# Kernel optimization log

Hardware: AMD Instinct MI355X
Metric: run time of the kernel (lower is better)

## Reference

```python
import jax, jax.numpy as jnp
import numpy as np

T, B, I, H, L, O = 512, 64, 128, 512, 2, 256


def _lstm_layer(x, Wih, Whh, b):
    """One LSTM layer over time. x:[T,B,in] -> (ys:[T,B,H], hT:[B,H], cT:[B,H]).
    PyTorch gate order: i, f, g, o. Zero initial state (module's zero buffers)."""
    Hs = Whh.shape[1]
    # Precompute input contribution for all timesteps (one big GEMM).
    xg = jnp.einsum('tbi,gi->tbg', x, Wih) + b  # [T,B,4H]

    def step(carry, xt):
        h, c = carry
        g = xt + h @ Whh.T  # [B,4H]
        i, f, gg, o = jnp.split(g, 4, axis=-1)
        c = jax.nn.sigmoid(f) * c + jax.nn.sigmoid(i) * jnp.tanh(gg)
        h = jax.nn.sigmoid(o) * jnp.tanh(c)
        return (h, c), h

    h0 = jnp.zeros((x.shape[1], Hs), x.dtype)
    (hT, cT), ys = jax.lax.scan(step, (h0, h0), xg)
    return ys, hT, cT


def setup_inputs() -> dict:
    key = jax.random.key(0)
    ks = jax.random.split(key, 9)
    s = 1.0 / np.sqrt(H)  # torch default uniform(-1/sqrt(H), 1/sqrt(H)) scale
    u = lambda k, shp: jax.random.uniform(k, shp, jnp.float32, -s, s)
    return {
        'x': jax.random.normal(ks[0], (T, B, I), jnp.float32),
        'W_ih0': u(ks[1], (4 * H, I)),
        'W_hh0': u(ks[2], (4 * H, H)),
        'b0': u(ks[3], (4 * H,)),  # b_ih + b_hh combined
        'W_ih1': u(ks[4], (4 * H, H)),
        'W_hh1': u(ks[5], (4 * H, H)),
        'b1': u(ks[6], (4 * H,)),
        'fc_w': u(ks[7], (O, H)),
        'fc_b': u(ks[8], (O,)),
    }


def reference(x, W_ih0, W_hh0, b0, W_ih1, W_hh1, b1, fc_w, fc_b):
    y0, h0, c0 = _lstm_layer(x, W_ih0, W_hh0, b0)
    y1, h1, c1 = _lstm_layer(y0, W_ih1, W_hh1, b1)
    fc = jnp.einsum('tbh,oh->tbo', y1, fc_w) + fc_b  # fused output projection
    hN = jnp.stack([h0, h1])  # [L,B,H]
    cN = jnp.stack([c0, c1])
    return fc, (hN, cN)
```

## Files before the change

kernel.cpp:

```cpp
#include <hip/hip_runtime.h>
#include <hip/hip_bf16.h>

#define T_SEQ 512
#define BATCH 64
#define IN0   128
#define HID   512
#define OUTF  256
#define G4    (4*HID)
#define NWG_L 64
#define FSTR  32

typedef __attribute__((ext_vector_type(8))) short short8;
typedef __attribute__((ext_vector_type(4))) float f32x4;
typedef unsigned short u16;
typedef unsigned long long u64;

__device__ __forceinline__ float sigmoidf_(float x) { return 1.f / (1.f + __expf(-x)); }
__device__ __forceinline__ float tanhf_(float x)    { return 1.f - 2.f / (1.f + __expf(2.f * x)); }

__device__ __forceinline__ u16 f2bf(float f) {
    union { float f; unsigned u; } a; a.f = f;
    unsigned u = a.u;
    return (u16)((u + 0x7fffu + ((u >> 16) & 1u)) >> 16);
}

template<int LAYER>
__device__ __forceinline__ void poll_all(const unsigned* fo, const unsigned* fd,
                                         int lane, unsigned to, unsigned td) {
    const unsigned* po = fo + (size_t)lane * FSTR;
    const unsigned* pd = fd + (size_t)lane * FSTR;
    unsigned it = 0;
    for (;;) {
        bool ok = true;
        if (to)
            ok = __hip_atomic_load(po, __ATOMIC_RELAXED, __HIP_MEMORY_SCOPE_AGENT) >= to;
        if (LAYER == 1)
            ok = ok && (__hip_atomic_load(pd, __ATOMIC_RELAXED, __HIP_MEMORY_SCOPE_AGENT) >= td);
        if (__all((int)ok)) return;
        if (it < 6) __builtin_amdgcn_s_sleep(1);
        else        __builtin_amdgcn_s_sleep(16);
        if ((++it & 1023u) == 0u)
            (void)__hip_atomic_load(po, __ATOMIC_ACQUIRE, __HIP_MEMORY_SCOPE_AGENT);
    }
}

__global__ void cvt_f32_bf16(const float* __restrict__ in, u16* __restrict__ out, int n4) {
    int i = blockIdx.x * blockDim.x + threadIdx.x;
    if (i < n4) {
        float4 v = reinterpret_cast<const float4*>(in)[i];
        ushort4 o;
        o.x = f2bf(v.x); o.y = f2bf(v.y); o.z = f2bf(v.z); o.w = f2bf(v.w);
        reinterpret_cast<ushort4*>(out)[i] = o;
    }
}

template<int LAYER>
__device__ __forceinline__ void run_layer(
    const u16* __restrict__ asrc,
    const u16* __restrict__ wih, const u16* __restrict__ whh,
    const float* __restrict__ bias,
    u16* __restrict__ ybuf,
    float* __restrict__ hNout, float* __restrict__ cNout,
    unsigned* flags_own, unsigned* flags_dep, int g,
    u16 (*lds_w)[32][512], float (*lds_g)[33], float (*lds_b)[16],
    unsigned (*lds_h)[4])
{
    constexpr int KIN = (LAYER == 0) ? IN0 : HID;
    constexpr int KS1 = KIN / 32;
    constexpr int KS  = KS1 + 16;

    const int tid  = threadIdx.x;
    const int lane = tid & 63;
    const int w    = tid >> 6;
    const int ubase = 8 * g;

    for (int idx = tid; idx < 2 * KS * 64; idx += 256) {
        int nt  = (idx >= KS * 64) ? 1 : 0;
        int rem = idx - nt * KS * 64;
        int ks = rem >> 6, s = rem & 63, q = s & 15, kq = s >> 4;
        int r = (q >> 2) * HID + ubase + 4 * nt + (q & 3);
        const u16* src = (ks < KS1)
            ? wih + (size_t)r * KIN + (size_t)ks * 32 + kq * 8
            : whh + (size_t)r * HID + (size_t)(ks - KS1) * 32 + kq * 8;
        *reinterpret_cast<uint4*>(&lds_w[nt][ks][s * 8]) =
            *reinterpret_cast<const uint4*>(src);
    }
    if (tid < 32) {
        int nt = tid >> 4, q = tid & 15;
        lds_b[nt][q] = bias[(q >> 2) * HID + ubase + 4 * nt + (q & 3)];
    }
    __syncthreads();

    const int pb  = tid & 63;
    const int pu2 = tid >> 6;
    float c0 = 0.f, c1 = 0.f;

    const int arow = 16 * w + (lane & 15);
    const int koff = (lane >> 4) * 8;

    for (int t = 0; t < T_SEQ; ++t) {
        f32x4 ac0[4] = {{0,0,0,0},{0,0,0,0},{0,0,0,0},{0,0,0,0}};
        f32x4 ac1[4] = {{0,0,0,0},{0,0,0,0},{0,0,0,0},{0,0,0,0}};

        if (LAYER == 0) {
            const u16* ap = asrc + ((size_t)t * BATCH + arow) * KIN + koff;
            short8 a[KS1];
            #pragma unroll
            for (int j = 0; j < KS1; ++j)
                a[j] = *reinterpret_cast<const short8*>(ap + j * 32);
            #pragma unroll
            for (int j = 0; j < KS1; ++j) {
                ac0[j & 3] = __builtin_amdgcn_mfma_f32_16x16x32_bf16(
                    a[j], *reinterpret_cast<const short8*>(&lds_w[0][j][lane * 8]), ac0[j & 3], 0, 0, 0);
                ac1[j & 3] = __builtin_amdgcn_mfma_f32_16x16x32_bf16(
                    a[j], *reinterpret_cast<const short8*>(&lds_w[1][j][lane * 8]), ac1[j & 3], 0, 0, 0);
            }
        }

        if (LAYER == 1 || t > 0)
            poll_all<LAYER>(flags_own, flags_dep, lane, (unsigned)t, (unsigned)(t + 1));

        if (LAYER == 1) {
            const u16* ap = asrc + ((size_t)t * BATCH + arow) * HID + koff;
            short8 ay[16];
            #pragma unroll
            for (int j = 0; j < 16; ++j)
                ay[j] = *reinterpret_cast<const short8*>(ap + j * 32);
            if (t > 0) {
                const u16* hp = ybuf + ((size_t)(t - 1) * BATCH + arow) * HID + koff;
                short8 ah[16];
                #pragma unroll
                for (int j = 0; j < 16; ++j)
                    ah[j] = *reinterpret_cast<const short8*>(hp + j * 32);
                #pragma unroll
                for (int j = 0; j < 16; ++j) {
                    ac0[j & 3] = __builtin_amdgcn_mfma_f32_16x16x32_bf16(
                        ay[j], *reinterpret_cast<const short8*>(&lds_w[0][j][lane * 8]), ac0[j & 3], 0, 0, 0);
                    ac1[j & 3] = __builtin_amdgcn_mfma_f32_16x16x32_bf16(
                        ay[j], *reinterpret_cast<const short8*>(&lds_w[1][j][lane * 8]), ac1[j & 3], 0, 0, 0);
                    ac0[j & 3] = __builtin_amdgcn_mfma_f32_16x16x32_bf16(
                        ah[j], *reinterpret_cast<const short8*>(&lds_w[0][KS1 + j][lane * 8]), ac0[j & 3], 0, 0, 0);
                    ac1[j & 3] = __builtin_amdgcn_mfma_f32_16x16x32_bf16(
                        ah[j], *reinterpret_cast<const short8*>(&lds_w[1][KS1 + j][lane * 8]), ac1[j & 3], 0, 0, 0);
                }
            } else {
                #pragma unroll
                for (int j = 0; j < 16; ++j) {
                    ac0[j & 3] = __builtin_amdgcn_mfma_f32_16x16x32_bf16(
                        ay[j], *reinterpret_cast<const short8*>(&lds_w[0][j][lane * 8]), ac0[j & 3], 0, 0, 0);
                    ac1[j & 3] = __builtin_amdgcn_mfma_f32_16x16x32_bf16(
                        ay[j], *reinterpret_cast<const short8*>(&lds_w[1][j][lane * 8]), ac1[j & 3], 0, 0, 0);
                }
            }
        } else if (t > 0) {
            const u16* hp = ybuf + ((size_t)(t - 1) * BATCH + arow) * HID + koff;
            short8 ah[16];
            #pragma unroll
            for (int j = 0; j < 16; ++j)
                ah[j] = *reinterpret_cast<const short8*>(hp + j * 32);
            #pragma unroll
            for (int j = 0; j < 16; ++j) {
                ac0[j & 3] = __builtin_amdgcn_mfma_f32_16x16x32_bf16(
                    ah[j], *reinterpret_cast<const short8*>(&lds_w[0][KS1 + j][lane * 8]), ac0[j & 3], 0, 0, 0);
                ac1[j & 3] = __builtin_amdgcn_mfma_f32_16x16x32_bf16(
                    ah[j], *reinterpret_cast<const short8*>(&lds_w[1][KS1 + j][lane * 8]), ac1[j & 3], 0, 0, 0);
            }
        }

        f32x4 s0 = (ac0[0] + ac0[1]) + (ac0[2] + ac0[3]);
        f32x4 s1 = (ac1[0] + ac1[1]) + (ac1[2] + ac1[3]);
        #pragma unroll
        for (int j = 0; j < 4; ++j) {
            int row = 16 * w + (lane >> 4) * 4 + j;
            lds_g[row][lane & 15]        = s0[j];
            lds_g[row][16 + (lane & 15)] = s1[j];
        }
        __syncthreads();

        {
            const int nt = pu2 >> 1;
            const int dq = (2 * pu2) & 3;
            const float* gr = &lds_g[pb][nt * 16];
            const float* br = lds_b[nt];
            float gi0 = sigmoidf_(gr[dq]      + br[dq]);
            float gf0 = sigmoidf_(gr[4 + dq]  + br[4 + dq]);
            float gg0 = tanhf_(   gr[8 + dq]  + br[8 + dq]);
            float go0 = sigmoidf_(gr[12 + dq] + br[12 + dq]);
            c0 = gf0 * c0 + gi0 * gg0;
            float h0v = go0 * tanhf_(c0);
            float gi1 = sigmoidf_(gr[dq + 1]      + br[dq + 1]);
            float gf1 = sigmoidf_(gr[4 + dq + 1]  + br[4 + dq + 1]);
            float gg1 = tanhf_(   gr[8 + dq + 1]  + br[8 + dq + 1]);
            float go1 = sigmoidf_(gr[12 + dq + 1] + br[12 + dq + 1]);
            c1 = gf1 * c1 + gi1 * gg1;
            float h1v = go1 * tanhf_(c1);

            lds_h[pb][pu2] = (unsigned)f2bf(h0v) | ((unsigned)f2bf(h1v) << 16);

            if (t == T_SEQ - 1) {
                const int u0 = ubase + 4 * nt + dq, u1 = u0 + 1;
                hNout[pb * HID + u0] = h0v;
                hNout[pb * HID + u1] = h1v;
                cNout[pb * HID + u0] = c0;
                cNout[pb * HID + u1] = c1;
            }
        }
        __syncthreads();

        if (w == (t & 3)) {
            uint4 hv = *reinterpret_cast<const uint4*>(&lds_h[lane][0]);
            u64 q0 = (u64)hv.x | ((u64)hv.y << 32);
            u64 q1 = (u64)hv.z | ((u64)hv.w << 32);
            u64* yp = reinterpret_cast<u64*>(
                ybuf + ((size_t)t * BATCH + lane) * HID + ubase);
            __hip_atomic_store(yp + 0, q0, __ATOMIC_RELAXED, __HIP_MEMORY_SCOPE_AGENT);
            __hip_atomic_store(yp + 1, q1, __ATOMIC_RELAXED, __HIP_MEMORY_SCOPE_AGENT);
            asm volatile("s_waitcnt vmcnt(0)" ::: "memory");
            if (lane == 0)
                __hip_atomic_store(flags_own + (size_t)g * FSTR, (unsigned)(t + 1),
                                   __ATOMIC_RELAXED, __HIP_MEMORY_SCOPE_AGENT);
        }
    }
}

__global__ __launch_bounds__(256, 1)
void lstm_fused(const u16* __restrict__ x_bf,
                const u16* __restrict__ wih0, const u16* __restrict__ whh0, const float* __restrict__ b0,
                const u16* __restrict__ wih1, const u16* __restrict__ whh1, const float* __restrict__ b1,
                u16* __restrict__ y0, u16* __restrict__ y1,
                float* __restrict__ hN, float* __restrict__ cN,
                unsigned* __restrict__ ctr)
{
    __shared__ __align__(16) u16 lds_w[2][32][512];
    __shared__ float lds_g[BATCH][33];
    __shared__ float lds_b[2][16];
    __shared__ __align__(16) unsigned lds_h[BATCH][4];

    unsigned* flags0 = ctr;
    unsigned* flags1 = ctr + NWG_L * FSTR;

    const int wgid = blockIdx.x;
    if (wgid < NWG_L) {
        run_layer<0>(x_bf, wih0, whh0, b0, y0, hN, cN,
                     flags0, flags0, wgid, lds_w, lds_g, lds_b, lds_h);
    } else {
        run_layer<1>(y0, wih1, whh1, b1, y1, hN + BATCH * HID, cN + BATCH * HID,
                     flags1, flags0, wgid - NWG_L, lds_w, lds_g, lds_b, lds_h);
    }
}

__global__ __launch_bounds__(256)
void fc_kernel(const u16* __restrict__ y1, const u16* __restrict__ fcw,
               const float* __restrict__ fcb, float* __restrict__ out)
{
    const int tid  = threadIdx.x;
    const int lane = tid & 63;
    const int wgid = blockIdx.x * 4 + (tid >> 6);
    const int nq   = wgid & 3;
    const int mt0  = wgid >> 2;

    for (int j = 0; j < 8; ++j) {
        int mt = mt0 + j * 256;
        f32x4 acc[4] = {{0,0,0,0},{0,0,0,0},{0,0,0,0},{0,0,0,0}};
        const u16* arow = y1 + ((size_t)mt * 16 + (lane & 15)) * HID + (lane >> 4) * 8;
        #pragma unroll
        for (int ks = 0; ks < 16; ++ks) {
            short8 a = *reinterpret_cast<const short8*>(arow + ks * 32);
            #pragma unroll
            for (int nt = 0; nt < 4; ++nt) {
                const u16* brow = fcw + ((size_t)(nq * 64 + nt * 16 + (lane & 15))) * HID
                                      + ks * 32 + (lane >> 4) * 8;
                short8 b = *reinterpret_cast<const short8*>(brow);
                acc[nt] = __builtin_amdgcn_mfma_f32_16x16x32_bf16(a, b, acc[nt], 0, 0, 0);
            }
        }
        #pragma unroll
        for (int nt = 0; nt < 4; ++nt) {
            int col = nq * 64 + nt * 16 + (lane & 15);
            float bb = fcb[col];
            #pragma unroll
            for (int jj = 0; jj < 4; ++jj) {
                int row = mt * 16 + (lane >> 4) * 4 + jj;
                out[(size_t)row * OUTF + col] = acc[nt][jj] + bb;
            }
        }
    }
}

extern "C" void kernel_launch(void* const* d_in, const int* in_sizes, int n_in,
                              void* d_out, int out_size, void* d_ws, size_t ws_size,
                              hipStream_t stream)
{
    const float* x    = (const float*)d_in[0];
    const float* wih0 = (const float*)d_in[1];
    const float* whh0 = (const float*)d_in[2];
    const float* b0   = (const float*)d_in[3];
    const float* wih1 = (const float*)d_in[4];
    const float* whh1 = (const float*)d_in[5];
    const float* b1   = (const float*)d_in[6];
    const float* fcw  = (const float*)d_in[7];
    const float* fcb  = (const float*)d_in[8];
    float* out = (float*)d_out;

    const size_t flag_bytes = (size_t)2 * NWG_L * FSTR * 4;

    char* ws = (char*)d_ws;
    size_t off = 0;
    unsigned* ctr = (unsigned*)ws;                    off += flag_bytes;
    u16* x_bf    = (u16*)(ws + off);                  off += (size_t)T_SEQ * BATCH * IN0 * 2;
    u16* wih0_bf = (u16*)(ws + off);                  off += (size_t)G4 * IN0 * 2;
    u16* whh0_bf = (u16*)(ws + off);                  off += (size_t)G4 * HID * 2;
    u16* wih1_bf = (u16*)(ws + off);                  off += (size_t)G4 * HID * 2;
    u16* whh1_bf = (u16*)(ws + off);                  off += (size_t)G4 * HID * 2;
    u16* fcw_bf  = (u16*)(ws + off);                  off += (size_t)OUTF * HID * 2;
    u16* y0      = (u16*)(ws + off);                  off += (size_t)T_SEQ * BATCH * HID * 2;
    u16* y1      = (u16*)(ws + off);                  off += (size_t)T_SEQ * BATCH * HID * 2;

    hipMemsetAsync(ctr, 0, flag_bytes, stream);

    auto conv = [&](const float* in, u16* o, int n) {
        int n4 = n / 4;
        cvt_f32_bf16<<<(n4 + 255) / 256, 256, 0, stream>>>(in, o, n4);
    };
    conv(x,    x_bf,    T_SEQ * BATCH * IN0);
    conv(wih0, wih0_bf, G4 * IN0);
    conv(whh0, whh0_bf, G4 * HID);
    conv(wih1, wih1_bf, G4 * HID);
    conv(whh1, whh1_bf, G4 * HID);
    conv(fcw,  fcw_bf,  OUTF * HID);

    float* outFC = out;
    float* hN = out + (size_t)T_SEQ * BATCH * OUTF;
    float* cN = hN + 2 * BATCH * HID;

    lstm_fused<<<2 * NWG_L, 256, 0, stream>>>(x_bf, wih0_bf, whh0_bf, b0,
                                              wih1_bf, whh1_bf, b1,
                                              y0, y1, hN, cN, ctr);
    fc_kernel<<<256, 256, 0, stream>>>(y1, fcw_bf, fcb, outFC);
}
```

Measured before the change: 3.651 ms.

## Add dedicated fifth wavefront to publish hidden state and signal flags

Launches 320 threads per workgroup. The extra wave copies the previous step's hidden-state tile from a now double-buffered LDS buffer to global memory and raises the progress flag, while the four compute waves start the next step's input MFMAs and polling. This removes the store-and-signal work from the compute waves' critical path. The polling backoff is also shortened (longer fast-spin phase, shorter long sleep). The extra wave adds scheduling pressure on the CU, and the cross-workgroup dependency still serializes steps, so the benefit may be limited.

```diff
diff --git a/kernel.cpp b/kernel.cpp
--- a/kernel.cpp
+++ b/kernel.cpp
@@ -9,6 +9,7 @@
 #define G4    (4*HID)
 #define NWG_L 64
 #define FSTR  32
+#define NTHR  320
 
 typedef __attribute__((ext_vector_type(8))) short short8;
 typedef __attribute__((ext_vector_type(4))) float f32x4;
@@ -37,8 +38,8 @@
         if (LAYER == 1)
             ok = ok && (__hip_atomic_load(pd, __ATOMIC_RELAXED, __HIP_MEMORY_SCOPE_AGENT) >= td);
         if (__all((int)ok)) return;
-        if (it < 6) __builtin_amdgcn_s_sleep(1);
-        else        __builtin_amdgcn_s_sleep(16);
+        if (it < 8) __builtin_amdgcn_s_sleep(1);
+        else        __builtin_amdgcn_s_sleep(8);
         if ((++it & 1023u) == 0u)
             (void)__hip_atomic_load(po, __ATOMIC_ACQUIRE, __HIP_MEMORY_SCOPE_AGENT);
     }
@@ -57,13 +58,13 @@
 template<int LAYER>
 __device__ __forceinline__ void run_layer(
     const u16* __restrict__ asrc,
-    const u16* __restrict__ wih, const u16* __restrict__ whh,
+    const u16* __restrict__ wihb, const u16* __restrict__ whhb,
     const float* __restrict__ bias,
     u16* __restrict__ ybuf,
     float* __restrict__ hNout, float* __restrict__ cNout,
     unsigned* flags_own, unsigned* flags_dep, int g,
     u16 (*lds_w)[32][512], float (*lds_g)[33], float (*lds_b)[16],
-    unsigned (*lds_h)[4])
+    unsigned (*lds_h)[BATCH][4])
 {
     constexpr int KIN = (LAYER == 0) ? IN0 : HID;
     constexpr int KS1 = KIN / 32;
@@ -74,14 +75,14 @@
     const int w    = tid >> 6;
     const int ubase = 8 * g;
 
-    for (int idx = tid; idx < 2 * KS * 64; idx += 256) {
+    for (int idx = tid; idx < 2 * KS * 64; idx += NTHR) {
         int nt  = (idx >= KS * 64) ? 1 : 0;
         int rem = idx - nt * KS * 64;
         int ks = rem >> 6, s = rem & 63, q = s & 15, kq = s >> 4;
         int r = (q >> 2) * HID + ubase + 4 * nt + (q & 3);
         const u16* src = (ks < KS1)
-            ? wih + (size_t)r * KIN + (size_t)ks * 32 + kq * 8
-            : whh + (size_t)r * HID + (size_t)(ks - KS1) * 32 + kq * 8;
+            ? wihb + (size_t)r * KIN + (size_t)ks * 32 + kq * 8
+            : whhb + (size_t)r * HID + (size_t)(ks - KS1) * 32 + kq * 8;
         *reinterpret_cast<uint4*>(&lds_w[nt][ks][s * 8]) =
             *reinterpret_cast<const uint4*>(src);
     }
@@ -102,31 +103,73 @@
         f32x4 ac0[4] = {{0,0,0,0},{0,0,0,0},{0,0,0,0},{0,0,0,0}};
         f32x4 ac1[4] = {{0,0,0,0},{0,0,0,0},{0,0,0,0},{0,0,0,0}};
 
-        if (LAYER == 0) {
-            const u16* ap = asrc + ((size_t)t * BATCH + arow) * KIN + koff;
-            short8 a[KS1];
-            #pragma unroll
-            for (int j = 0; j < KS1; ++j)
-                a[j] = *reinterpret_cast<const short8*>(ap + j * 32);
-            #pragma unroll
-            for (int j = 0; j < KS1; ++j) {
-                ac0[j & 3] = __builtin_amdgcn_mfma_f32_16x16x32_bf16(
-                    a[j], *reinterpret_cast<const short8*>(&lds_w[0][j][lane * 8]), ac0[j & 3], 0, 0, 0);
-                ac1[j & 3] = __builtin_amdgcn_mfma_f32_16x16x32_bf16(
-                    a[j], *reinterpret_cast<const short8*>(&lds_w[1][j][lane * 8]), ac1[j & 3], 0, 0, 0);
-            }
-        }
-
-        if (LAYER == 1 || t > 0)
-            poll_all<LAYER>(flags_own, flags_dep, lane, (unsigned)t, (unsigned)(t + 1));
-
-        if (LAYER == 1) {
-            const u16* ap = asrc + ((size_t)t * BATCH + arow) * HID + koff;
-            short8 ay[16];
-            #pragma unroll
-            for (int j = 0; j < 16; ++j)
-                ay[j] = *reinterpret_cast<const short8*>(ap + j * 32);
+        if (w == 4) {
             if (t > 0) {
+                const int s = t - 1;
+                const unsigned* hr = lds_h[s & 1][lane];
+                u64 q0 = (u64)hr[0] | ((u64)hr[1] << 32);
+                u64 q1 = (u64)hr[2] | ((u64)hr[3] << 32);
+                u64* yp = reinterpret_cast<u64*>(
+                    ybuf + ((size_t)s * BATCH + lane) * HID + ubase);
+                __hip_atomic_store(yp + 0, q0, __ATOMIC_RELAXED, __HIP_MEMORY_SCOPE_AGENT);
+                __hip_atomic_store(yp + 1, q1, __ATOMIC_RELAXED, __HIP_MEMORY_SCOPE_AGENT);
+                asm volatile("s_waitcnt vmcnt(0)" ::: "memory");
+                if (lane == 0)
+                    __hip_atomic_store(flags_own + (size_t)g * FSTR, (unsigned)t,
+                                       __ATOMIC_RELAXED, __HIP_MEMORY_SCOPE_AGENT);
+            }
+        } else {
+            if (LAYER == 0) {
+                const u16* ap = asrc + ((size_t)t * BATCH + arow) * KIN + koff;
+                short8 a[KS1];
+                #pragma unroll
+                for (int j = 0; j < KS1; ++j)
+                    a[j] = *reinterpret_cast<const short8*>(ap + j * 32);
+                #pragma unroll
+                for (int j = 0; j < KS1; ++j) {
+                    ac0[j & 3] = __builtin_amdgcn_mfma_f32_16x16x32_bf16(
+                        a[j], *reinterpret_cast<const short8*>(&lds_w[0][j][lane * 8]), ac0[j & 3], 0, 0, 0);
+                    ac1[j & 3] = __builtin_amdgcn_mfma_f32_16x16x32_bf16(
+                        a[j], *reinterpret_cast<const short8*>(&lds_w[1][j][lane * 8]), ac1[j & 3], 0, 0, 0);
+                }
+            }
+
+            if (LAYER == 1 || t > 0)
+                poll_all<LAYER>(flags_own, flags_dep, lane, (unsigned)t, (unsigned)(t + 1));
+
+            if (LAYER == 1) {
+                const u16* ap = asrc + ((size_t)t * BATCH + arow) * HID + koff;
+                short8 ay[16];
+                #pragma unroll
+                for (int j = 0; j < 16; ++j)
+                    ay[j] = *reinterpret_cast<const short8*>(ap + j * 32);
+                if (t > 0) {
+                    const u16* hp = ybuf + ((size_t)(t - 1) * BATCH + arow) * HID + koff;
+                    short8 ah[16];
+                    #pragma unroll
+                    for (int j = 0; j < 16; ++j)
+                        ah[j] = *reinterpret_cast<const short8*>(hp + j * 32);
+                    #pragma unroll
+                    for (int j = 0; j < 16; ++j) {
+                        ac0[j & 3] = __builtin_amdgcn_mfma_f32_16x16x32_bf16(
+                            ay[j], *reinterpret_cast<const short8*>(&lds_w[0][j][lane * 8]), ac0[j & 3], 0, 0, 0);
+                        ac1[j & 3] = __builtin_amdgcn_mfma_f32_16x16x32_bf16(
+                            ay[j], *reinterpret_cast<const short8*>(&lds_w[1][j][lane * 8]), ac1[j & 3], 0, 0, 0);
+                        ac0[j & 3] = __builtin_amdgcn_mfma_f32_16x16x32_bf16(
+                            ah[j], *reinterpret_cast<const short8*>(&lds_w[0][KS1 + j][lane * 8]), ac0[j & 3], 0, 0, 0);
+                        ac1[j & 3] = __builtin_amdgcn_mfma_f32_16x16x32_bf16(
+                            ah[j], *reinterpret_cast<const short8*>(&lds_w[1][KS1 + j][lane * 8]), ac1[j & 3], 0, 0, 0);
+                    }
+                } else {
+                    #pragma unroll
+                    for (int j = 0; j < 16; ++j) {
+                        ac0[j & 3] = __builtin_amdgcn_mfma_f32_16x16x32_bf16(
+                            ay[j], *reinterpret_cast<const short8*>(&lds_w[0][j][lane * 8]), ac0[j & 3], 0, 0, 0);
+                        ac1[j & 3] = __builtin_amdgcn_mfma_f32_16x16x32_bf16(
+                            ay[j], *reinterpret_cast<const short8*>(&lds_w[1][j][lane * 8]), ac1[j & 3], 0, 0, 0);
+                    }
+                }
+            } else if (t > 0) {
                 const u16* hp = ybuf + ((size_t)(t - 1) * BATCH + arow) * HID + koff;
                 short8 ah[16];
                 #pragma unroll
@@ -134,50 +177,25 @@
                     ah[j] = *reinterpret_cast<const short8*>(hp + j * 32);
                 #pragma unroll
                 for (int j = 0; j < 16; ++j) {
-                    ac0[j & 3] = __builtin_amdgcn_mfma_f32_16x16x32_bf16(
-                        ay[j], *reinterpret_cast<const short8*>(&lds_w[0][j][lane * 8]), ac0[j & 3], 0, 0, 0);
-                    ac1[j & 3] = __builtin_amdgcn_mfma_f32_16x16x32_bf16(
-                        ay[j], *reinterpret_cast<const short8*>(&lds_w[1][j][lane * 8]), ac1[j & 3], 0, 0, 0);
                     ac0[j & 3] = __builtin_amdgcn_mfma_f32_16x16x32_bf16(
                         ah[j], *reinterpret_cast<const short8*>(&lds_w[0][KS1 + j][lane * 8]), ac0[j & 3], 0, 0, 0);
                     ac1[j & 3] = __builtin_amdgcn_mfma_f32_16x16x32_bf16(
                         ah[j], *reinterpret_cast<const short8*>(&lds_w[1][KS1 + j][lane * 8]), ac1[j & 3], 0, 0, 0);
                 }
-            } else {
-                #pragma unroll
-                for (int j = 0; j < 16; ++j) {
-                    ac0[j & 3] = __builtin_amdgcn_mfma_f32_16x16x32_bf16(
-                        ay[j], *reinterpret_cast<const short8*>(&lds_w[0][j][lane * 8]), ac0[j & 3], 0, 0, 0);
-                    ac1[j & 3] = __builtin_amdgcn_mfma_f32_16x16x32_bf16(
-                        ay[j], *reinterpret_cast<const short8*>(&lds_w[1][j][lane * 8]), ac1[j & 3], 0, 0, 0);
-                }
-            }
-        } else if (t > 0) {
-            const u16* hp = ybuf + ((size_t)(t - 1) * BATCH + arow) * HID + koff;
-            short8 ah[16];
+            }
+
+            f32x4 s0 = (ac0[0] + ac0[1]) + (ac0[2] + ac0[3]);
+            f32x4 s1 = (ac1[0] + ac1[1]) + (ac1[2] + ac1[3]);
             #pragma unroll
-            for (int j = 0; j < 16; ++j)
-                ah[j] = *reinterpret_cast<const short8*>(hp + j * 32);
-            #pragma unroll
-            for (int j = 0; j < 16; ++j) {
-                ac0[j & 3] = __builtin_amdgcn_mfma_f32_16x16x32_bf16(
-                    ah[j], *reinterpret_cast<const short8*>(&lds_w[0][KS1 + j][lane * 8]), ac0[j & 3], 0, 0, 0);
-                ac1[j & 3] = __builtin_amdgcn_mfma_f32_16x16x32_bf16(
-                    ah[j], *reinterpret_cast<const short8*>(&lds_w[1][KS1 + j][lane * 8]), ac1[j & 3], 0, 0, 0);
-            }
-        }
-
-        f32x4 s0 = (ac0[0] + ac0[1]) + (ac0[2] + ac0[3]);
-        f32x4 s1 = (ac1[0] + ac1[1]) + (ac1[2] + ac1[3]);
-        #pragma unroll
-        for (int j = 0; j < 4; ++j) {
-            int row = 16 * w + (lane >> 4) * 4 + j;
-            lds_g[row][lane & 15]        = s0[j];
-            lds_g[row][16 + (lane & 15)] = s1[j];
+            for (int j = 0; j < 4; ++j) {
+                int row = 16 * w + (lane >> 4) * 4 + j;
+                lds_g[row][lane & 15]        = s0[j];
+                lds_g[row][16 + (lane & 15)] = s1[j];
+            }
         }
         __syncthreads();
 
-        {
+        if (w < 4) {
             const int nt = pu2 >> 1;
             const int dq = (2 * pu2) & 3;
             const float* gr = &lds_g[pb][nt * 16];
@@ -195,7 +213,7 @@
             c1 = gf1 * c1 + gi1 * gg1;
             float h1v = go1 * tanhf_(c1);
 
-            lds_h[pb][pu2] = (unsigned)f2bf(h0v) | ((unsigned)f2bf(h1v) << 16);
+            lds_h[t & 1][pb][pu2] = (unsigned)f2bf(h0v) | ((unsigned)f2bf(h1v) << 16);
 
             if (t == T_SEQ - 1) {
                 const int u0 = ubase + 4 * nt + dq, u1 = u0 + 1;
@@ -206,24 +224,25 @@
             }
         }
         __syncthreads();
-
-        if (w == (t & 3)) {
-            uint4 hv = *reinterpret_cast<const uint4*>(&lds_h[lane][0]);
-            u64 q0 = (u64)hv.x | ((u64)hv.y << 32);
-            u64 q1 = (u64)hv.z | ((u64)hv.w << 32);
-            u64* yp = reinterpret_cast<u64*>(
-                ybuf + ((size_t)t * BATCH + lane) * HID + ubase);
-            __hip_atomic_store(yp + 0, q0, __ATOMIC_RELAXED, __HIP_MEMORY_SCOPE_AGENT);
-            __hip_atomic_store(yp + 1, q1, __ATOMIC_RELAXED, __HIP_MEMORY_SCOPE_AGENT);
-            asm volatile("s_waitcnt vmcnt(0)" ::: "memory");
-            if (lane == 0)
-                __hip_atomic_store(flags_own + (size_t)g * FSTR, (unsigned)(t + 1),
-                                   __ATOMIC_RELAXED, __HIP_MEMORY_SCOPE_AGENT);
-        }
-    }
-}
-
-__global__ __launch_bounds__(256, 1)
+    }
+
+    if (w == 4) {
+        const int s = T_SEQ - 1;
+        const unsigned* hr = lds_h[s & 1][lane];
+        u64 q0 = (u64)hr[0] | ((u64)hr[1] << 32);
+        u64 q1 = (u64)hr[2] | ((u64)hr[3] << 32);
+        u64* yp = reinterpret_cast<u64*>(
+            ybuf + ((size_t)s * BATCH + lane) * HID + ubase);
+        __hip_atomic_store(yp + 0, q0, __ATOMIC_RELAXED, __HIP_MEMORY_SCOPE_AGENT);
+        __hip_atomic_store(yp + 1, q1, __ATOMIC_RELAXED, __HIP_MEMORY_SCOPE_AGENT);
+        asm volatile("s_waitcnt vmcnt(0)" ::: "memory");
+        if (lane == 0)
+            __hip_atomic_store(flags_own + (size_t)g * FSTR, (unsigned)T_SEQ,
+                               __ATOMIC_RELAXED, __HIP_MEMORY_SCOPE_AGENT);
+    }
+}
+
+__global__ __launch_bounds__(NTHR, 1)
 void lstm_fused(const u16* __restrict__ x_bf,
                 const u16* __restrict__ wih0, const u16* __restrict__ whh0, const float* __restrict__ b0,
                 const u16* __restrict__ wih1, const u16* __restrict__ whh1, const float* __restrict__ b1,
@@ -234,7 +253,7 @@
     __shared__ __align__(16) u16 lds_w[2][32][512];
     __shared__ float lds_g[BATCH][33];
     __shared__ float lds_b[2][16];
-    __shared__ __align__(16) unsigned lds_h[BATCH][4];
+    __shared__ __align__(16) unsigned lds_h[2][BATCH][4];
 
     unsigned* flags0 = ctr;
     unsigned* flags1 = ctr + NWG_L * FSTR;
@@ -333,8 +352,8 @@
     float* hN = out + (size_t)T_SEQ * BATCH * OUTF;
     float* cN = hN + 2 * BATCH * HID;
 
-    lstm_fused<<<2 * NWG_L, 256, 0, stream>>>(x_bf, wih0_bf, whh0_bf, b0,
-                                              wih1_bf, whh1_bf, b1,
-                                              y0, y1, hN, cN, ctr);
+    lstm_fused<<<2 * NWG_L, NTHR, 0, stream>>>(x_bf, wih0_bf, whh0_bf, b0,
+                                               wih1_bf, whh1_bf, b1,
+                                               y0, y1, hN, cN, ctr);
     fc_kernel<<<256, 256, 0, stream>>>(y1, fcw_bf, fcb, outFC);
 }
```

After: 3.780 ms. 1.04x slower.
